# Optimization experiments

Hardware: AMD Instinct MI355X
Metric: run time of the kernel (lower is better)

## Reference

```python
import jax, jax.numpy as jnp
import numpy as np

N_NODES = 50000
N_EDGES = 800000
IN_DIM = 128
HID = 32
HEADS = 4
OUT_DIM = 64
NEG_SLOPE = 0.2


def _glorot(key, shape):
    fan = shape[0] + shape[-1] if len(shape) > 1 else shape[-1]
    lim = jnp.sqrt(6.0 / fan)
    return jax.random.uniform(key, shape, jnp.float32, -lim, lim)


def setup_inputs() -> dict:
    key = jax.random.key(0)
    ks = jax.random.split(key, 10)
    x = jax.random.normal(ks[0], (N_NODES, IN_DIM), jnp.float32)
    edge_index = jax.random.randint(ks[1], (2, N_EDGES), 0, N_NODES, jnp.int32)
    # layer 1: in=IN_DIM, heads=HEADS, out=HID, concat
    W1 = _glorot(ks[2], (IN_DIM, HEADS * HID))
    a_src1 = _glorot(ks[3], (HEADS, HID))
    a_dst1 = _glorot(ks[4], (HEADS, HID))
    b1 = jnp.zeros((HEADS * HID,), jnp.float32)
    # layer 2: in=HEADS*HID, heads=1, out=OUT_DIM, mean
    W2 = _glorot(ks[5], (HEADS * HID, OUT_DIM))
    a_src2 = _glorot(ks[6], (1, OUT_DIM))
    a_dst2 = _glorot(ks[7], (1, OUT_DIM))
    b2 = jnp.zeros((OUT_DIM,), jnp.float32)
    return {"x": x, "edge_index": edge_index, "W1": W1, "a_src1": a_src1,
            "a_dst1": a_dst1, "b1": b1, "W2": W2, "a_src2": a_src2,
            "a_dst2": a_dst2, "b2": b2}


def gat_conv(x, src, dst, W, a_src, a_dst, bias, heads, out_ch, concat, num_nodes):
    # x: [N, in]; src/dst: [E] (self-loops already included)
    h = (x @ W).reshape(num_nodes, heads, out_ch)          # [N, H, F]
    alpha_s = jnp.einsum('nhf,hf->nh', h, a_src)           # [N, H]
    alpha_d = jnp.einsum('nhf,hf->nh', h, a_dst)
    e = alpha_s[src] + alpha_d[dst]                        # [E, H]
    e = jnp.where(e >= 0, e, NEG_SLOPE * e)                # leaky relu
    # segment softmax over destination neighborhoods
    e_max = jax.ops.segment_max(e, dst, num_segments=num_nodes)
    ex = jnp.exp(e - e_max[dst])
    denom = jax.ops.segment_sum(ex, dst, num_segments=num_nodes)
    alpha = ex / (denom[dst] + 1e-16)                      # [E, H]
    msg = h[src] * alpha[:, :, None]                       # [E, H, F]
    out = jax.ops.segment_sum(msg, dst, num_segments=num_nodes)  # [N, H, F]
    if concat:
        out = out.reshape(num_nodes, heads * out_ch)
    else:
        out = out.mean(axis=1)
    return out + bias


def reference(x, edge_index, W1, a_src1, a_dst1, b1, W2, a_src2, a_dst2, b2):
    n = x.shape[0]
    # PyG GATConv default add_self_loops=True
    loop = jnp.arange(n, dtype=edge_index.dtype)
    src = jnp.concatenate([edge_index[0], loop])
    dst = jnp.concatenate([edge_index[1], loop])
    h = gat_conv(x, src, dst, W1, a_src1, a_dst1, b1, HEADS, HID, True, n)
    h = jax.nn.relu(h)
    out = gat_conv(h, src, dst, W2, a_src2, a_dst2, b2, 1, OUT_DIM, False, n)
    return out
```

## Files before the change

kernel.cpp:

```cpp
#include <hip/hip_runtime.h>
#include <hip/hip_fp16.h>
#include <math.h>


#define NEG_SLOPE 0.2f
#define CAP 64

__device__ __forceinline__ float lrelu_exp(float e) {
    e = (e >= 0.f) ? e : NEG_SLOPE * e;
    return __expf(e);
}

__global__ __launch_bounds__(256) void build_kernel(
    const float* __restrict__ x, const float* __restrict__ W1,
    const float* __restrict__ a_src1, const float* __restrict__ a_dst1,
    __half* __restrict__ h1h, float* __restrict__ as1, float* __restrict__ ad1,
    const int* __restrict__ src, const int* __restrict__ dst,
    int* __restrict__ deg, unsigned short* __restrict__ col,
    int N, int E, int Gg) {
    __shared__ float Ws[32 * 128];
    __shared__ float xs[64 * 32];
    const int tid = threadIdx.x;

    if (blockIdx.x >= Gg) {
        const int base = (blockIdx.x - Gg) * 2048 + tid * 8;
        int s[8], d[8];
        if (base + 8 <= E) {
            int4 a0 = *(const int4*)&src[base];
            int4 a1 = *(const int4*)&src[base + 4];
            int4 c0 = *(const int4*)&dst[base];
            int4 c1 = *(const int4*)&dst[base + 4];
            s[0]=a0.x; s[1]=a0.y; s[2]=a0.z; s[3]=a0.w;
            s[4]=a1.x; s[5]=a1.y; s[6]=a1.z; s[7]=a1.w;
            d[0]=c0.x; d[1]=c0.y; d[2]=c0.z; d[3]=c0.w;
            d[4]=c1.x; d[5]=c1.y; d[6]=c1.z; d[7]=c1.w;
        } else {
#pragma unroll
            for (int u = 0; u < 8; ++u) {
                int i = base + u;
                if (i < E) { s[u] = src[i]; d[u] = dst[i]; }
                else       { s[u] = -1;     d[u] = -1; }
            }
        }
        int p[8];
#pragma unroll
        for (int u = 0; u < 8; ++u)
            if (d[u] >= 0) p[u] = atomicAdd(&deg[d[u]], 1);
#pragma unroll
        for (int u = 0; u < 8; ++u)
            if (d[u] >= 0 && p[u] < CAP)
                col[d[u] * CAP + p[u]] = (unsigned short)s[u];
        return;
    }

    const int tf = tid & 31;
    const int tn = tid >> 5;
    const int nb = blockIdx.x * 64;
    float acc[8][4];
#pragma unroll
    for (int i = 0; i < 8; ++i)
#pragma unroll
        for (int j = 0; j < 4; ++j) acc[i][j] = 0.f;

    for (int kc = 0; kc < 128; kc += 32) {
#pragma unroll
        for (int l = 0; l < 4; ++l) {
            int idx = tid + l * 256;
            int k = idx >> 5, f4 = idx & 31;
            *(float4*)&Ws[k * 128 + f4 * 4] =
                *(const float4*)&W1[(kc + k) * 128 + f4 * 4];
        }
#pragma unroll
        for (int l = 0; l < 2; ++l) {
            int idx = tid + l * 256;
            int n = idx >> 3, j = idx & 7;
            int gn = nb + n; if (gn >= N) gn = N - 1;
            *(float4*)&xs[n * 32 + j * 4] =
                *(const float4*)&x[gn * 128 + kc + j * 4];
        }
        __syncthreads();
#pragma unroll
        for (int k = 0; k < 32; ++k) {
            float4 w = *(const float4*)&Ws[k * 128 + tf * 4];
#pragma unroll
            for (int i = 0; i < 8; ++i) {
                float xv = xs[(tn * 8 + i) * 32 + k];
                acc[i][0] += xv * w.x; acc[i][1] += xv * w.y;
                acc[i][2] += xv * w.z; acc[i][3] += xv * w.w;
            }
        }
        __syncthreads();
    }
    float4 asv = *(const float4*)&a_src1[tf * 4];
    float4 adv = *(const float4*)&a_dst1[tf * 4];
    const int head = tf >> 3;
    const int lane8 = tf & 7;
#pragma unroll
    for (int i = 0; i < 8; ++i) {
        int n = nb + tn * 8 + i;
        if (n < N) {
            __half2 p0 = __floats2half2_rn(acc[i][0], acc[i][1]);
            __half2 p1 = __floats2half2_rn(acc[i][2], acc[i][3]);
            uint2 pk;
            pk.x = *(unsigned*)&p0;
            pk.y = *(unsigned*)&p1;
            *(uint2*)&h1h[(size_t)n * 128 + tf * 4] = pk;
        }
        float s = acc[i][0]*asv.x + acc[i][1]*asv.y + acc[i][2]*asv.z + acc[i][3]*asv.w;
        float d = acc[i][0]*adv.x + acc[i][1]*adv.y + acc[i][2]*adv.z + acc[i][3]*adv.w;
        s += __shfl_down(s, 4); d += __shfl_down(d, 4);
        s += __shfl_down(s, 2); d += __shfl_down(d, 2);
        s += __shfl_down(s, 1); d += __shfl_down(d, 1);
        if (lane8 == 0 && n < N) { as1[n * 4 + head] = s; ad1[n * 4 + head] = d; }
    }
}

__global__ __launch_bounds__(256) void agg1mm_kernel(
    const __half2* __restrict__ h1h2, const float* __restrict__ as1,
    const float* __restrict__ ad1, const float* __restrict__ b1,
    const float* __restrict__ W2, const float* __restrict__ a_src2,
    const float* __restrict__ a_dst2, const int* __restrict__ deg,
    const unsigned short* __restrict__ col,
    __half* __restrict__ h2h, float* __restrict__ as2, float* __restrict__ ad2,
    int N) {
    __shared__ float wls[4][4][68];
    __shared__ int   cls[4][64];
    __shared__ float hrs[4][128];
    __shared__ float part[16][64];
    const int tid = threadIdx.x;
    const int w = tid >> 6;
    const int lane = tid & 63;
    const int d = blockIdx.x * 4 + w;

    if (d < N) {
        const int hsel = lane >> 4;
        const float4 ad4 = *(const float4*)&ad1[4 * d];
        const float4 asd = *(const float4*)&as1[4 * d];
        const float adh = (hsel == 0) ? ad4.x : (hsel == 1) ? ad4.y
                        : (hsel == 2) ? ad4.z : ad4.w;
        const float ash = (hsel == 0) ? asd.x : (hsel == 1) ? asd.y
                        : (hsel == 2) ? asd.z : asd.w;
        const int dg = min(deg[d], CAP);
        const int dgp = (dg + 15) & ~15;
        const int beg = d * CAP;

        if (lane < dgp) {
            if (lane < dg) {
                int s = (int)col[beg + lane];
                cls[w][lane] = s;
                float4 a4 = *(const float4*)&as1[4 * s];
                wls[w][0][lane] = lrelu_exp(a4.x + ad4.x);
                wls[w][1][lane] = lrelu_exp(a4.y + ad4.y);
                wls[w][2][lane] = lrelu_exp(a4.z + ad4.z);
                wls[w][3][lane] = lrelu_exp(a4.w + ad4.w);
            } else {
                cls[w][lane] = 0;
                wls[w][0][lane] = 0.f;
                wls[w][1][lane] = 0.f;
                wls[w][2][lane] = 0.f;
                wls[w][3][lane] = 0.f;
            }
        }

        float wself = lrelu_exp(ash + adh);
        float2 vself = __half22float2(h1h2[((unsigned)d << 6) | (unsigned)lane]);
        float den = wself, accx = wself * vself.x, accy = wself * vself.y;

        for (int jj = 0; jj < dgp; jj += 16) {
            int4 c0 = *(const int4*)&cls[w][jj];
            int4 c1 = *(const int4*)&cls[w][jj + 4];
            int4 c2 = *(const int4*)&cls[w][jj + 8];
            int4 c3 = *(const int4*)&cls[w][jj + 12];
            int ss[16] = {c0.x, c0.y, c0.z, c0.w, c1.x, c1.y, c1.z, c1.w,
                          c2.x, c2.y, c2.z, c2.w, c3.x, c3.y, c3.z, c3.w};
            __half2 v[16];
#pragma unroll
            for (int u = 0; u < 16; ++u)
                v[u] = h1h2[(((unsigned)ss[u]) << 6) | (unsigned)lane];
            float4 w0 = *(const float4*)&wls[w][hsel][jj];
            float4 w1 = *(const float4*)&wls[w][hsel][jj + 4];
            float4 w2 = *(const float4*)&wls[w][hsel][jj + 8];
            float4 w3 = *(const float4*)&wls[w][hsel][jj + 12];
            float wt[16] = {w0.x, w0.y, w0.z, w0.w, w1.x, w1.y, w1.z, w1.w,
                            w2.x, w2.y, w2.z, w2.w, w3.x, w3.y, w3.z, w3.w};
#pragma unroll
            for (int u = 0; u < 16; ++u) {
                float2 vf = __half22float2(v[u]);
                den += wt[u];
                accx += wt[u] * vf.x;
                accy += wt[u] * vf.y;
            }
        }
        const float inv = 1.f / (den + 1e-16f);
        float2 bv = *(const float2*)&b1[lane * 2];
        float2 o;
        o.x = fmaxf(accx * inv + bv.x, 0.f);
        o.y = fmaxf(accy * inv + bv.y, 0.f);
        *(float2*)&hrs[w][lane * 2] = o;
    } else {
        hrs[w][lane * 2] = 0.f;
        hrs[w][lane * 2 + 1] = 0.f;
    }
    __syncthreads();

    float p0 = 0.f, p1 = 0.f, p2 = 0.f, p3 = 0.f;
#pragma unroll
    for (int kk = 0; kk < 32; kk += 4) {
        const int k = w * 32 + kk;
        float4 h0 = *(const float4*)&hrs[0][k];
        float4 h1 = *(const float4*)&hrs[1][k];
        float4 h2 = *(const float4*)&hrs[2][k];
        float4 h3 = *(const float4*)&hrs[3][k];
        float wv0 = W2[(k + 0) * 64 + lane];
        float wv1 = W2[(k + 1) * 64 + lane];
        float wv2 = W2[(k + 2) * 64 + lane];
        float wv3 = W2[(k + 3) * 64 + lane];
        p0 += h0.x * wv0 + h0.y * wv1 + h0.z * wv2 + h0.w * wv3;
        p1 += h1.x * wv0 + h1.y * wv1 + h1.z * wv2 + h1.w * wv3;
        p2 += h2.x * wv0 + h2.y * wv1 + h2.z * wv2 + h2.w * wv3;
        p3 += h3.x * wv0 + h3.y * wv1 + h3.z * wv2 + h3.w * wv3;
    }
    part[w * 4 + 0][lane] = p0;
    part[w * 4 + 1][lane] = p1;
    part[w * 4 + 2][lane] = p2;
    part[w * 4 + 3][lane] = p3;
    __syncthreads();

    if (d < N) {
        float h2f = part[0 * 4 + w][lane] + part[1 * 4 + w][lane] +
                    part[2 * 4 + w][lane] + part[3 * 4 + w][lane];
        h2h[((unsigned)d << 6) | (unsigned)lane] = __float2half(h2f);
        float s = h2f * a_src2[lane];
        float dv = h2f * a_dst2[lane];
        s += __shfl_down(s, 32); dv += __shfl_down(dv, 32);
        s += __shfl_down(s, 16); dv += __shfl_down(dv, 16);
        s += __shfl_down(s, 8);  dv += __shfl_down(dv, 8);
        s += __shfl_down(s, 4);  dv += __shfl_down(dv, 4);
        s += __shfl_down(s, 2);  dv += __shfl_down(dv, 2);
        s += __shfl_down(s, 1);  dv += __shfl_down(dv, 1);
        if (lane == 0) { as2[d] = s; ad2[d] = dv; }
    }
}

__global__ __launch_bounds__(256) void agg2_kernel(
    const __half* __restrict__ h2h, const float* __restrict__ as2,
    const float* __restrict__ ad2, const float* __restrict__ b2,
    const int* __restrict__ deg, const unsigned short* __restrict__ col,
    float* __restrict__ out, int N) {
    __shared__ int   cls[4][64];
    __shared__ float wl[4][64];
    const int lane = threadIdx.x & 63;
    const int w = threadIdx.x >> 6;
    const int d = blockIdx.x * 4 + w;
    if (d >= N) return;
    const int dg = min(deg[d], CAP);
    const int dgp = (dg + 15) & ~15;
    const int beg = d * CAP;
    const float adv = ad2[d];

    float wself = lrelu_exp(as2[d] + adv);
    float den = wself;
    float acc = wself * __half2float(h2h[((unsigned)d << 6) | (unsigned)lane]);

    if (lane < dgp) {
        if (lane < dg) {
            int s = (int)col[beg + lane];
            cls[w][lane] = s;
            wl[w][lane] = lrelu_exp(as2[s] + adv);
        } else {
            cls[w][lane] = 0;
            wl[w][lane] = 0.f;
        }
    }

    for (int jj = 0; jj < dgp; jj += 16) {
        int4 c0 = *(const int4*)&cls[w][jj];
        int4 c1 = *(const int4*)&cls[w][jj + 4];
        int4 c2 = *(const int4*)&cls[w][jj + 8];
        int4 c3 = *(const int4*)&cls[w][jj + 12];
        int ss[16] = {c0.x, c0.y, c0.z, c0.w, c1.x, c1.y, c1.z, c1.w,
                      c2.x, c2.y, c2.z, c2.w, c3.x, c3.y, c3.z, c3.w};
        __half v[16];
#pragma unroll
        for (int u = 0; u < 16; ++u)
            v[u] = h2h[(((unsigned)ss[u]) << 6) | (unsigned)lane];
        float4 w0 = *(const float4*)&wl[w][jj];
        float4 w1 = *(const float4*)&wl[w][jj + 4];
        float4 w2 = *(const float4*)&wl[w][jj + 8];
        float4 w3 = *(const float4*)&wl[w][jj + 12];
        float wt[16] = {w0.x, w0.y, w0.z, w0.w, w1.x, w1.y, w1.z, w1.w,
                        w2.x, w2.y, w2.z, w2.w, w3.x, w3.y, w3.z, w3.w};
#pragma unroll
        for (int u = 0; u < 16; ++u) {
            den += wt[u];
            acc += wt[u] * __half2float(v[u]);
        }
    }
    out[(size_t)d * 64 + lane] = acc / (den + 1e-16f) + b2[lane];
}

extern "C" void kernel_launch(void* const* d_in, const int* in_sizes, int n_in,
                              void* d_out, int out_size, void* d_ws, size_t ws_size,
                              hipStream_t stream) {
    const float* x      = (const float*)d_in[0];
    const int*   eidx   = (const int*)d_in[1];
    const float* W1     = (const float*)d_in[2];
    const float* a_src1 = (const float*)d_in[3];
    const float* a_dst1 = (const float*)d_in[4];
    const float* b1     = (const float*)d_in[5];
    const float* W2     = (const float*)d_in[6];
    const float* a_src2 = (const float*)d_in[7];
    const float* a_dst2 = (const float*)d_in[8];
    const float* b2     = (const float*)d_in[9];
    float* out = (float*)d_out;

    const int N = in_sizes[0] / 128;
    const int E = in_sizes[1] / 2;

    const int* src = eidx;
    const int* dst = eidx + E;

    float* ws_f = (float*)d_ws;
    float* as1 = ws_f;
    float* ad1 = as1 + (size_t)N * 4;
    float* as2 = ad1 + (size_t)N * 4;
    float* ad2 = as2 + (size_t)N;
    __half* h1h = (__half*)(ad2 + (size_t)N);
    __half* h2h = h1h + (size_t)N * 128;
    int* deg = (int*)(h2h + (size_t)N * 64);
    unsigned short* col = (unsigned short*)(deg + N);

    const int Gg = (N + 63) / 64;
    const int Gs = (E + 2047) / 2048;

    hipMemsetAsync(deg, 0, (size_t)N * sizeof(int), stream);

    build_kernel<<<Gg + Gs, 256, 0, stream>>>(x, W1, a_src1, a_dst1,
                                              h1h, as1, ad1,
                                              src, dst, deg, col, N, E, Gg);

    agg1mm_kernel<<<(N + 3) / 4, 256, 0, stream>>>(
        (const __half2*)h1h, as1, ad1, b1, W2, a_src2, a_dst2,
        deg, col, h2h, as2, ad2, N);

    agg2_kernel<<<(N + 3) / 4, 256, 0, stream>>>(h2h, as2, ad2, b2,
                                                 deg, col, out, N);
}
```

Measured before the change: 199.2 us.

## Use packed half2 FMA aggregation with max-subtracted softmax and partitioned edge scatter

Both aggregation kernels now compute the max-subtracted softmax weights with wavefront shuffle reductions. The weights are stored as half2 in shared memory, and the gather-accumulate runs with packed __hfma2 in fp16, with the denominator computed separately in fp32. This is meant to halve the ALU work per gathered neighbour; the max subtraction keeps the fp16 weights in range, but fp16 accumulation risks precision loss. The edge-scatter blocks are replicated eight times, and each copy handles only destinations in its own node partition, which likely improves atomic and column-write locality at the cost of reading the edge list eight times.

Result: slower. 218.0 us (+9.4%).

```diff
diff --git a/kernel.cpp b/kernel.cpp
--- a/kernel.cpp
+++ b/kernel.cpp
@@ -6,9 +6,8 @@
 #define NEG_SLOPE 0.2f
 #define CAP 64
 
-__device__ __forceinline__ float lrelu_exp(float e) {
-    e = (e >= 0.f) ? e : NEG_SLOPE * e;
-    return __expf(e);
+__device__ __forceinline__ float lrelu(float e) {
+    return (e >= 0.f) ? e : NEG_SLOPE * e;
 }
 
 __global__ __launch_bounds__(256) void build_kernel(
@@ -23,7 +22,12 @@
     const int tid = threadIdx.x;
 
     if (blockIdx.x >= Gg) {
-        const int base = (blockIdx.x - Gg) * 2048 + tid * 8;
+        const int sb = blockIdx.x - Gg;
+        const int part = sb & 7;
+        const int stripe = sb >> 3;
+        const int psz = (N + 7) / 8;
+        const int dlo = part * psz;
+        const int base = stripe * 2048 + tid * 8;
         int s[8], d[8];
         if (base + 8 <= E) {
             int4 a0 = *(const int4*)&src[base];
@@ -39,17 +43,16 @@
             for (int u = 0; u < 8; ++u) {
                 int i = base + u;
                 if (i < E) { s[u] = src[i]; d[u] = dst[i]; }
-                else       { s[u] = -1;     d[u] = -1; }
+                else       { s[u] = -1;     d[u] = -(1 << 30); }
             }
         }
-        int p[8];
-#pragma unroll
-        for (int u = 0; u < 8; ++u)
-            if (d[u] >= 0) p[u] = atomicAdd(&deg[d[u]], 1);
-#pragma unroll
-        for (int u = 0; u < 8; ++u)
-            if (d[u] >= 0 && p[u] < CAP)
-                col[d[u] * CAP + p[u]] = (unsigned short)s[u];
+#pragma unroll
+        for (int u = 0; u < 8; ++u) {
+            if ((unsigned)(d[u] - dlo) < (unsigned)psz) {
+                int p = atomicAdd(&deg[d[u]], 1);
+                if (p < CAP) col[d[u] * CAP + p] = (unsigned short)s[u];
+            }
+        }
         return;
     }
 
@@ -123,10 +126,10 @@
     const unsigned short* __restrict__ col,
     __half* __restrict__ h2h, float* __restrict__ as2, float* __restrict__ ad2,
     int N) {
-    __shared__ float wls[4][4][68];
-    __shared__ int   cls[4][64];
-    __shared__ float hrs[4][128];
-    __shared__ float part[16][64];
+    __shared__ __half2 wls[4][4][68];
+    __shared__ int     cls[4][64];
+    __shared__ float   hrs[4][128];
+    __shared__ float   part[16][64];
     const int tid = threadIdx.x;
     const int w = tid >> 6;
     const int lane = tid & 63;
@@ -136,35 +139,73 @@
         const int hsel = lane >> 4;
         const float4 ad4 = *(const float4*)&ad1[4 * d];
         const float4 asd = *(const float4*)&as1[4 * d];
-        const float adh = (hsel == 0) ? ad4.x : (hsel == 1) ? ad4.y
-                        : (hsel == 2) ? ad4.z : ad4.w;
-        const float ash = (hsel == 0) ? asd.x : (hsel == 1) ? asd.y
-                        : (hsel == 2) ? asd.z : asd.w;
         const int dg = min(deg[d], CAP);
         const int dgp = (dg + 15) & ~15;
         const int beg = d * CAP;
 
+        float4 l4 = make_float4(-1e30f, -1e30f, -1e30f, -1e30f);
+        if (lane < dg) {
+            int s = (int)col[beg + lane];
+            cls[w][lane] = s;
+            float4 a4 = *(const float4*)&as1[4 * s];
+            l4.x = lrelu(a4.x + ad4.x);
+            l4.y = lrelu(a4.y + ad4.y);
+            l4.z = lrelu(a4.z + ad4.z);
+            l4.w = lrelu(a4.w + ad4.w);
+        } else if (lane < dgp) {
+            cls[w][lane] = 0;
+        }
+        float4 ls4;
+        ls4.x = lrelu(asd.x + ad4.x);
+        ls4.y = lrelu(asd.y + ad4.y);
+        ls4.z = lrelu(asd.z + ad4.z);
+        ls4.w = lrelu(asd.w + ad4.w);
+
+        float4 m4 = l4;
+#pragma unroll
+        for (int off = 32; off; off >>= 1) {
+            m4.x = fmaxf(m4.x, __shfl_xor(m4.x, off));
+            m4.y = fmaxf(m4.y, __shfl_xor(m4.y, off));
+            m4.z = fmaxf(m4.z, __shfl_xor(m4.z, off));
+            m4.w = fmaxf(m4.w, __shfl_xor(m4.w, off));
+        }
+        m4.x = fmaxf(m4.x, ls4.x); m4.y = fmaxf(m4.y, ls4.y);
+        m4.z = fmaxf(m4.z, ls4.z); m4.w = fmaxf(m4.w, ls4.w);
+
+        float4 w4 = make_float4(0.f, 0.f, 0.f, 0.f);
+        if (lane < dg) {
+            w4.x = __expf(l4.x - m4.x);
+            w4.y = __expf(l4.y - m4.y);
+            w4.z = __expf(l4.z - m4.z);
+            w4.w = __expf(l4.w - m4.w);
+        }
         if (lane < dgp) {
-            if (lane < dg) {
-                int s = (int)col[beg + lane];
-                cls[w][lane] = s;
-                float4 a4 = *(const float4*)&as1[4 * s];
-                wls[w][0][lane] = lrelu_exp(a4.x + ad4.x);
-                wls[w][1][lane] = lrelu_exp(a4.y + ad4.y);
-                wls[w][2][lane] = lrelu_exp(a4.z + ad4.z);
-                wls[w][3][lane] = lrelu_exp(a4.w + ad4.w);
-            } else {
-                cls[w][lane] = 0;
-                wls[w][0][lane] = 0.f;
-                wls[w][1][lane] = 0.f;
-                wls[w][2][lane] = 0.f;
-                wls[w][3][lane] = 0.f;
-            }
-        }
-
-        float wself = lrelu_exp(ash + adh);
-        float2 vself = __half22float2(h1h2[((unsigned)d << 6) | (unsigned)lane]);
-        float den = wself, accx = wself * vself.x, accy = wself * vself.y;
+            wls[w][0][lane] = __float2half2_rn(w4.x);
+            wls[w][1][lane] = __float2half2_rn(w4.y);
+            wls[w][2][lane] = __float2half2_rn(w4.z);
+            wls[w][3][lane] = __float2half2_rn(w4.w);
+        }
+
+        float4 ds = w4;
+#pragma unroll
+        for (int off = 32; off; off >>= 1) {
+            ds.x += __shfl_xor(ds.x, off);
+            ds.y += __shfl_xor(ds.y, off);
+            ds.z += __shfl_xor(ds.z, off);
+            ds.w += __shfl_xor(ds.w, off);
+        }
+        float4 ws4;
+        ws4.x = __expf(ls4.x - m4.x);
+        ws4.y = __expf(ls4.y - m4.y);
+        ws4.z = __expf(ls4.z - m4.z);
+        ws4.w = __expf(ls4.w - m4.w);
+        float den   = (hsel == 0) ? ds.x + ws4.x : (hsel == 1) ? ds.y + ws4.y
+                    : (hsel == 2) ? ds.z + ws4.z : ds.w + ws4.w;
+        float wself = (hsel == 0) ? ws4.x : (hsel == 1) ? ws4.y
+                    : (hsel == 2) ? ws4.z : ws4.w;
+
+        __half2 vself = h1h2[((unsigned)d << 6) | (unsigned)lane];
+        __half2 acc2 = __hmul2(__float2half2_rn(wself), vself);
 
         for (int jj = 0; jj < dgp; jj += 16) {
             int4 c0 = *(const int4*)&cls[w][jj];
@@ -177,25 +218,21 @@
 #pragma unroll
             for (int u = 0; u < 16; ++u)
                 v[u] = h1h2[(((unsigned)ss[u]) << 6) | (unsigned)lane];
-            float4 w0 = *(const float4*)&wls[w][hsel][jj];
-            float4 w1 = *(const float4*)&wls[w][hsel][jj + 4];
-            float4 w2 = *(const float4*)&wls[w][hsel][jj + 8];
-            float4 w3 = *(const float4*)&wls[w][hsel][jj + 12];
-            float wt[16] = {w0.x, w0.y, w0.z, w0.w, w1.x, w1.y, w1.z, w1.w,
-                            w2.x, w2.y, w2.z, w2.w, w3.x, w3.y, w3.z, w3.w};
-#pragma unroll
-            for (int u = 0; u < 16; ++u) {
-                float2 vf = __half22float2(v[u]);
-                den += wt[u];
-                accx += wt[u] * vf.x;
-                accy += wt[u] * vf.y;
-            }
-        }
+            __half2 wt[16];
+            *(uint4*)&wt[0]  = *(const uint4*)&wls[w][hsel][jj];
+            *(uint4*)&wt[4]  = *(const uint4*)&wls[w][hsel][jj + 4];
+            *(uint4*)&wt[8]  = *(const uint4*)&wls[w][hsel][jj + 8];
+            *(uint4*)&wt[12] = *(const uint4*)&wls[w][hsel][jj + 12];
+#pragma unroll
+            for (int u = 0; u < 16; ++u)
+                acc2 = __hfma2(wt[u], v[u], acc2);
+        }
+        float2 af = __half22float2(acc2);
         const float inv = 1.f / (den + 1e-16f);
         float2 bv = *(const float2*)&b1[lane * 2];
         float2 o;
-        o.x = fmaxf(accx * inv + bv.x, 0.f);
-        o.y = fmaxf(accy * inv + bv.y, 0.f);
+        o.x = fmaxf(af.x * inv + bv.x, 0.f);
+        o.y = fmaxf(af.y * inv + bv.y, 0.f);
         *(float2*)&hrs[w][lane * 2] = o;
     } else {
         hrs[w][lane * 2] = 0.f;
@@ -247,8 +284,8 @@
     const float* __restrict__ ad2, const float* __restrict__ b2,
     const int* __restrict__ deg, const unsigned short* __restrict__ col,
     float* __restrict__ out, int N) {
-    __shared__ int   cls[4][64];
-    __shared__ float wl[4][64];
+    __shared__ int     cls[4][64];
+    __shared__ __half2 wl[4][68];
     const int lane = threadIdx.x & 63;
     const int w = threadIdx.x >> 6;
     const int d = blockIdx.x * 4 + w;
@@ -258,21 +295,36 @@
     const int beg = d * CAP;
     const float adv = ad2[d];
 
-    float wself = lrelu_exp(as2[d] + adv);
-    float den = wself;
-    float acc = wself * __half2float(h2h[((unsigned)d << 6) | (unsigned)lane]);
-
-    if (lane < dgp) {
-        if (lane < dg) {
-            int s = (int)col[beg + lane];
-            cls[w][lane] = s;
-            wl[w][lane] = lrelu_exp(as2[s] + adv);
-        } else {
-            cls[w][lane] = 0;
-            wl[w][lane] = 0.f;
-        }
-    }
-
+    float l = -1e30f;
+    if (lane < dg) {
+        int s = (int)col[beg + lane];
+        cls[w][lane] = s;
+        l = lrelu(as2[s] + adv);
+    } else if (lane < dgp) {
+        cls[w][lane] = 0;
+    }
+    const float lself = lrelu(as2[d] + adv);
+
+    float m = l;
+#pragma unroll
+    for (int off = 32; off; off >>= 1) m = fmaxf(m, __shfl_xor(m, off));
+    m = fmaxf(m, lself);
+
+    float wlf = (lane < dg) ? __expf(l - m) : 0.f;
+    if (lane < dgp) wl[w][lane] = __float2half2_rn(wlf);
+
+    float den = wlf;
+#pragma unroll
+    for (int off = 32; off; off >>= 1) den += __shfl_xor(den, off);
+    const float wself = __expf(lself - m);
+    den += wself;
+
+    __half2 sv;
+    sv.x = h2h[((unsigned)d << 6) | (unsigned)lane];
+    sv.y = __float2half(0.f);
+    __half2 acc2 = __hmul2(__float2half2_rn(wself), sv);
+
+    const unsigned short* h2u = (const unsigned short*)h2h;
     for (int jj = 0; jj < dgp; jj += 16) {
         int4 c0 = *(const int4*)&cls[w][jj];
         int4 c1 = *(const int4*)&cls[w][jj + 4];
@@ -280,22 +332,22 @@
         int4 c3 = *(const int4*)&cls[w][jj + 12];
         int ss[16] = {c0.x, c0.y, c0.z, c0.w, c1.x, c1.y, c1.z, c1.w,
                       c2.x, c2.y, c2.z, c2.w, c3.x, c3.y, c3.z, c3.w};
-        __half v[16];
+        unsigned vv[16];
 #pragma unroll
         for (int u = 0; u < 16; ++u)
-            v[u] = h2h[(((unsigned)ss[u]) << 6) | (unsigned)lane];
-        float4 w0 = *(const float4*)&wl[w][jj];
-        float4 w1 = *(const float4*)&wl[w][jj + 4];
-        float4 w2 = *(const float4*)&wl[w][jj + 8];
-        float4 w3 = *(const float4*)&wl[w][jj + 12];
-        float wt[16] = {w0.x, w0.y, w0.z, w0.w, w1.x, w1.y, w1.z, w1.w,
-                        w2.x, w2.y, w2.z, w2.w, w3.x, w3.y, w3.z, w3.w};
+            vv[u] = (unsigned)h2u[(((unsigned)ss[u]) << 6) | (unsigned)lane];
+        __half2 wt[16];
+        *(uint4*)&wt[0]  = *(const uint4*)&wl[w][jj];
+        *(uint4*)&wt[4]  = *(const uint4*)&wl[w][jj + 4];
+        *(uint4*)&wt[8]  = *(const uint4*)&wl[w][jj + 8];
+        *(uint4*)&wt[12] = *(const uint4*)&wl[w][jj + 12];
 #pragma unroll
         for (int u = 0; u < 16; ++u) {
-            den += wt[u];
-            acc += wt[u] * __half2float(v[u]);
-        }
-    }
+            __half2 v = *(__half2*)&vv[u];
+            acc2 = __hfma2(wt[u], v, acc2);
+        }
+    }
+    float acc = __half2float(acc2.x);
     out[(size_t)d * 64 + lane] = acc / (den + 1e-16f) + b2[lane];
 }
 
@@ -331,7 +383,7 @@
     unsigned short* col = (unsigned short*)(deg + N);
 
     const int Gg = (N + 63) / 64;
-    const int Gs = (E + 2047) / 2048;
+    const int Gs = ((E + 2047) / 2048) * 8;
 
     hipMemsetAsync(deg, 0, (size_t)N * sizeof(int), stream);
 
```
